# Performance work log

Hardware: AMD Instinct MI355X
Metric: run time of the kernel (lower is better)

The kernel has to match this reference:

```python
import jax, jax.numpy as jnp
import numpy as np

B, S, E, HD = 32, 1024, 768, 64
NUM_IMAGE_PATCHES = 49


def setup_inputs() -> dict:
    key = jax.random.key(0)
    ks = jax.random.split(key, 9)
    w = 0.02
    return {
        "decoder_sequence": jax.random.normal(ks[0], (B, S, E), dtype=jnp.float32),
        "Wq": jax.random.normal(ks[1], (E, HD), dtype=jnp.float32) * w,
        "bq": jnp.zeros((HD,), dtype=jnp.float32),
        "Wk": jax.random.normal(ks[2], (E, HD), dtype=jnp.float32) * w,
        "bk": jnp.zeros((HD,), dtype=jnp.float32),
        "Wv": jax.random.normal(ks[3], (E, HD), dtype=jnp.float32) * w,
        "bv": jnp.zeros((HD,), dtype=jnp.float32),
        "input_sequence_length": 975,
        "padding_mask": jax.random.randint(ks[4], (B, 1, S), 0, 2).astype(bool),
    }


def reference(decoder_sequence, Wq, bq, Wk, bk, Wv, bv, input_sequence_length, padding_mask):
    # single-head projections: [B,S,E] @ [E,HD] -> [B,S,HD]
    Q = decoder_sequence @ Wq + bq
    K = decoder_sequence @ Wk + bk
    V = decoder_sequence @ Wv + bv

    scores = jnp.einsum('bid,bjd->bij', Q, K) / jnp.sqrt(jnp.float32(HD))

    # mask: image-patch rows (i < 49) fully unmasked; text region is causal
    # (mask[49:,49:] = triu(-inf, diag=1)), i.e. -inf where i >= 49 and j > i.
    i = jnp.arange(S)[:, None]
    j = jnp.arange(S)[None, :]
    causal_bad = (i >= NUM_IMAGE_PATCHES) & (j > i)  # [S,S]
    scores = jnp.where(causal_bad[None, :, :], -jnp.inf, scores)

    # padding mask on keys, broadcast over queries: [B,1,S] -> [B,S,S]
    scores = jnp.where(padding_mask, -jnp.inf, scores)

    A = jax.nn.softmax(scores, axis=-1)
    H = jnp.einsum('bij,bjd->bid', A, V)
    return H
```

## Files before the change

kernel.cpp:

```cpp
#include <hip/hip_runtime.h>
#include <stdint.h>
#include <stddef.h>


typedef __attribute__((ext_vector_type(8))) short bf16x8;
typedef __attribute__((ext_vector_type(4))) float f32x4;

#define NIP 49
#define QSCALE 0.18033688011112042f

#define GLDS16(g, l)                                      \
  __builtin_amdgcn_global_load_lds(                       \
      (const __attribute__((address_space(1))) void*)(g), \
      (__attribute__((address_space(3))) void*)(l), 16, 0, 0)

__device__ __forceinline__ short f2b(float f) {
  union { float f; uint32_t u; } c; c.f = f;
  uint32_t u = c.u;
  uint32_t r = (u + 0x7fffu + ((u >> 16) & 1u)) >> 16;
  return (short)(uint16_t)r;
}

__device__ __forceinline__ uint32_t pk2(float lo, float hi) {
  uint32_t r;
  asm("v_cvt_pk_bf16_f32 %0, %1, %2" : "=v"(r) : "v"(lo), "v"(hi));
  return r;
}

__global__ __launch_bounds__(256) void wt_kernel(
    const float* __restrict__ Wq, const float* __restrict__ Wk,
    const float* __restrict__ Wv, const int* __restrict__ pad,
    short* __restrict__ Wt, float* __restrict__ padneg) {
  int idx = blockIdx.x * 256 + threadIdx.x;
  int n = idx / 768;
  int k = idx - n * 768;
  const float* W = (n < 64) ? Wq : (n < 128) ? Wk : Wv;
  Wt[idx] = f2b(W[(size_t)k * 64 + (n & 63)]);
  if (idx < 32768) padneg[idx] = pad[idx] ? -16384.f : 0.f;
}

__global__ __launch_bounds__(256, 3) void proj_kernel(
    const float* __restrict__ X, const float* __restrict__ bq,
    const float* __restrict__ bk, const float* __restrict__ bv,
    const short* __restrict__ Wt, short* __restrict__ Qg,
    short* __restrict__ Kg, short* __restrict__ Vt) {
  __shared__ short lW[2][2][192][32];
  const int tid = threadIdx.x;
  const int wid = tid >> 6, lane = tid & 63;
  const int l15 = lane & 15, q4 = lane >> 4;
  const int r0 = blockIdx.x * 64;
  const int sig = (l15 >> 1) & 3;

  const float* xrow = X + (size_t)(r0 + wid * 16 + l15) * 768;
  float4 xa[2][4];
  auto xload = [&](int slot, int st) {
    const int kb = st * 64 + q4 * 8;
#pragma unroll
    for (int h = 0; h < 2; ++h) {
      xa[slot][h * 2 + 0] = *(const float4*)(xrow + kb + h * 32);
      xa[slot][h * 2 + 1] = *(const float4*)(xrow + kb + h * 32 + 4);
    }
  };
  auto mkfrag = [&](int slot, int h) {
    union { uint32_t u[4]; bf16x8 v; } r;
    const float4 a = xa[slot][h * 2], b = xa[slot][h * 2 + 1];
    r.u[0] = pk2(a.x, a.y); r.u[1] = pk2(a.z, a.w);
    r.u[2] = pk2(b.x, b.y); r.u[3] = pk2(b.z, b.w);
    return r.v;
  };

  const int wr = lane >> 2;
  const int ws = (((lane & 3) ^ ((wr >> 1) & 3)) * 8);
  auto wlds = [&](int buf, int st) {
    const int kb = st * 64;
#pragma unroll
    for (int i = 0; i < 6; ++i) {
      const int fi = wid * 6 + i;
      const int j = fi >> 1, ks = fi & 1;
      GLDS16(Wt + (size_t)(j * 16 + wr) * 768 + kb + ks * 32 + ws,
             &lW[buf][ks][j * 16][0]);
    }
  };

  f32x4 acc[12];
#pragma unroll
  for (int c = 0; c < 12; ++c) acc[c] = (f32x4){0.f, 0.f, 0.f, 0.f};

  wlds(0, 0);
  __builtin_amdgcn_sched_barrier(0);
  xload(0, 0);
  xload(1, 1);
  asm volatile("s_waitcnt vmcnt(8) lgkmcnt(0)" ::: "memory");
  __builtin_amdgcn_s_barrier();

#pragma unroll
  for (int st = 0; st < 12; ++st) {
    const int cur = st & 1;
    if (st + 1 < 12) {
      wlds(cur ^ 1, st + 1);
      __builtin_amdgcn_sched_barrier(0);
    }
    const bf16x8 a0 = mkfrag(cur, 0);
    const bf16x8 a1 = mkfrag(cur, 1);
    if (st + 2 < 12) xload(cur, st + 2);
#pragma unroll
    for (int ks = 0; ks < 2; ++ks) {
      const bf16x8 a = ks ? a1 : a0;
#pragma unroll
      for (int c = 0; c < 12; ++c) {
        const bf16x8 bw =
            *(const bf16x8*)&lW[cur][ks][c * 16 + l15][(q4 ^ sig) * 8];
        acc[c] = __builtin_amdgcn_mfma_f32_16x16x32_bf16(a, bw, acc[c], 0, 0, 0);
      }
    }
    if (st + 2 < 12)
      asm volatile("s_waitcnt vmcnt(4) lgkmcnt(0)" ::: "memory");
    else
      asm volatile("s_waitcnt vmcnt(0) lgkmcnt(0)" ::: "memory");
    __builtin_amdgcn_s_barrier();
  }

  const int b = r0 >> 10, s0 = r0 & 1023;
#pragma unroll
  for (int c = 0; c < 12; ++c) {
    const int mtx = c >> 2;
    const int h = (c & 3) * 16 + l15;
    if (mtx < 2) {
      const float bias = (mtx == 0 ? bq : bk)[h];
      short* op = (mtx == 0) ? Qg : Kg;
#pragma unroll
      for (int rr = 0; rr < 4; ++rr) {
        int row = r0 + wid * 16 + q4 * 4 + rr;
        float v = acc[c][rr] + bias;
        if (mtx == 0) v *= QSCALE;
        op[(size_t)row * 64 + h] = f2b(v);
      }
    } else {
      const float bias = bv[h];
      uint2 sv;
      sv.x = pk2(acc[c][0] + bias, acc[c][1] + bias);
      sv.y = pk2(acc[c][2] + bias, acc[c][3] + bias);
      *(uint2*)(Vt + ((size_t)(b * 64 + h) << 10) + s0 + wid * 16 + q4 * 4) = sv;
    }
  }
}

__global__ __launch_bounds__(256, 2) void attn_kernel(
    const short* __restrict__ Qg, const short* __restrict__ Kg,
    const short* __restrict__ Vt, const float* __restrict__ padneg,
    float* __restrict__ out) {
  __shared__ short lK[2][2][128][32];
  __shared__ short lV[2][4][64][32];
  __shared__ short lOnes[16][32];

  const int b = blockIdx.x;
  const int level = blockIdx.y;
  const int t = (level == 0) ? 0 : 16 - level;
  const int tid = threadIdx.x;
  const int wid = tid >> 6, lane = tid & 63;
  const int l15 = lane & 15, q4 = lane >> 4;
  const int qs = t * 64;
  const size_t base = (size_t)b * 1024;
  const int nkt = (t == 0) ? 8 : (t / 2 + 1);

  {
    int i0 = tid, i1 = tid + 256;
    ((short*)lOnes)[i0] = ((i0 >> 5) == 0) ? (short)0x3F80 : (short)0;
    if (i1 < 512) ((short*)lOnes)[i1] = ((i1 >> 5) == 0) ? (short)0x3F80 : (short)0;
  }

  const short* qrow = Qg + (base + qs + wid * 16 + l15) * 64;
  bf16x8 bq0 = *(const bf16x8*)(qrow + q4 * 8);
  bf16x8 bq1 = *(const bf16x8*)(qrow + 32 + q4 * 8);
  const int qi = qs + wid * 16 + l15;

  const int sr = lane >> 2, sc = (lane & 3) * 8;
  auto wlds_tile = [&](int buf, int kt) {
    const int kb = kt * 128;
#pragma unroll
    for (int i = 0; i < 4; ++i) {
      const int dh = i & 1, krow = wid * 32 + (i >> 1) * 16;
      GLDS16(Kg + (base + kb + krow + sr) * 64 + dh * 32 + sc,
             &lK[buf][dh][krow][0]);
    }
#pragma unroll
    for (int kq = 0; kq < 4; ++kq) {
      GLDS16(Vt + ((size_t)(b * 64 + wid * 16 + sr) << 10) + kb + kq * 32 + sc,
             &lV[buf][kq][wid * 16][0]);
    }
  };

  float4 pnv[8];
  auto pnload = [&](int kt) {
#pragma unroll
    for (int c = 0; c < 8; ++c)
      pnv[c] = *(const float4*)(padneg + base + kt * 128 + c * 16 + q4 * 4);
  };

  pnload(0);
  wlds_tile(0, 0);
  __syncthreads();

  f32x4 o[5];
#pragma unroll
  for (int c = 0; c < 5; ++c) o[c] = (f32x4){0.f, 0.f, 0.f, 0.f};

  for (int kt = 0; kt < nkt; ++kt) {
    const int cur = kt & 1;
    const int kb = kt * 128;

    f32x4 s4[8];
#pragma unroll
    for (int c = 0; c < 8; ++c)
      s4[c] = (f32x4){pnv[c].x, pnv[c].y, pnv[c].z, pnv[c].w};

    if (kt + 1 < nkt) {
      wlds_tile(cur ^ 1, kt + 1);
      pnload(kt + 1);
    }

#pragma unroll
    for (int c = 0; c < 8; ++c) {
      bf16x8 a0 = *(const bf16x8*)&lK[cur][0][c * 16 + l15][q4 * 8];
      s4[c] = __builtin_amdgcn_mfma_f32_16x16x32_bf16(a0, bq0, s4[c], 0, 0, 0);
      bf16x8 a1 = *(const bf16x8*)&lK[cur][1][c * 16 + l15][q4 * 8];
      s4[c] = __builtin_amdgcn_mfma_f32_16x16x32_bf16(a1, bq1, s4[c], 0, 0, 0);
    }

    const bool diag = (t == 0) ? (kt == 0) : (kt == nkt - 1);
    const bool img = (t == 0 && kt > 0);
#pragma unroll
    for (int c = 0; c < 8; ++c) {
#pragma unroll
      for (int rr = 0; rr < 4; ++rr) {
        float pv = exp2f(fminf(s4[c][rr], 80.f));
        if (diag) {
          int j = kb + c * 16 + q4 * 4 + rr;
          if (qi >= NIP && j > qi) pv = 0.f;
        }
        if (img) {
          if (qi >= NIP) pv = 0.f;
        }
        s4[c][rr] = pv;
      }
    }

#pragma unroll
    for (int m = 0; m < 4; ++m) {
      uint32_t w0 = pk2(s4[2 * m][0], s4[2 * m][1]);
      uint32_t w1 = pk2(s4[2 * m][2], s4[2 * m][3]);
      uint32_t w2 = pk2(s4[2 * m + 1][0], s4[2 * m + 1][1]);
      uint32_t w3 = pk2(s4[2 * m + 1][2], s4[2 * m + 1][3]);
      asm("v_permlane32_swap_b32 %0, %1" : "+v"(w0), "+v"(w2));
      asm("v_permlane32_swap_b32 %0, %1" : "+v"(w1), "+v"(w3));
      asm("v_permlane16_swap_b32 %0, %1" : "+v"(w0), "+v"(w2));
      asm("v_permlane16_swap_b32 %0, %1" : "+v"(w1), "+v"(w3));
      union { uint32_t u[4]; bf16x8 v; } af;
      af.u[0] = w0; af.u[1] = w1; af.u[2] = w2; af.u[3] = w3;
#pragma unroll
      for (int c = 0; c < 5; ++c) {
        bf16x8 bv = (c < 4) ? *(const bf16x8*)&lV[cur][m][c * 16 + l15][q4 * 8]
                            : *(const bf16x8*)&lOnes[l15][q4 * 8];
        o[c] = __builtin_amdgcn_mfma_f32_16x16x32_bf16(af.v, bv, o[c], 0, 0, 0);
      }
    }
    __syncthreads();
  }

#pragma unroll
  for (int rr = 0; rr < 4; ++rr) {
    float l = __shfl(o[4][rr], lane & 48, 64);
    const float inv = (l > 0.f) ? 1.0f / l : 0.f;
    const size_t row = base + qs + wid * 16 + q4 * 4 + rr;
#pragma unroll
    for (int c = 0; c < 4; ++c)
      out[row * 64 + c * 16 + l15] = o[c][rr] * inv;
  }
}

extern "C" void kernel_launch(void* const* d_in, const int* in_sizes, int n_in,
                              void* d_out, int out_size, void* d_ws, size_t ws_size,
                              hipStream_t stream) {
  const float* X  = (const float*)d_in[0];
  const float* Wq = (const float*)d_in[1];
  const float* bq = (const float*)d_in[2];
  const float* Wk = (const float*)d_in[3];
  const float* bk = (const float*)d_in[4];
  const float* Wv = (const float*)d_in[5];
  const float* bv = (const float*)d_in[6];
  const int* pad  = (const int*)d_in[8];
  float* out = (float*)d_out;

  short* Qg = (short*)d_ws;
  short* Kg = Qg + 32768 * 64;
  short* Vt = Kg + 32768 * 64;
  short* Wt = Vt + 32768 * 64;
  float* padneg = (float*)(Wt + 147456);

  wt_kernel<<<576, 256, 0, stream>>>(Wq, Wk, Wv, pad, Wt, padneg);
  proj_kernel<<<512, 256, 0, stream>>>(X, bq, bk, bv, Wt, Qg, Kg, Vt);
  attn_kernel<<<dim3(32, 16), 256, 0, stream>>>(Qg, Kg, Vt, padneg, out);
}
```

Measured before the change: 198.1 us.

## Load projection weights directly from global memory instead of LDS staging

The projection kernel no longer stages the transposed weight tiles in shared memory with async global-to-LDS loads, double buffering and barriers. Each wave now reads its bf16 weight fragments straight from global memory, relying on L1/L2 caching because every block reuses the same small weight matrix. The weight transpose kernel is rewritten to read the source coalesced and scatter-write the transpose, and the occupancy hint on launch_bounds is dropped. This removes LDS traffic and block-wide synchronisation but exposes global load latency inside the MFMA loop with no explicit prefetch.

```diff
diff --git a/kernel.cpp b/kernel.cpp
--- a/kernel.cpp
+++ b/kernel.cpp
@@ -32,24 +32,23 @@
     const float* __restrict__ Wv, const int* __restrict__ pad,
     short* __restrict__ Wt, float* __restrict__ padneg) {
   int idx = blockIdx.x * 256 + threadIdx.x;
-  int n = idx / 768;
-  int k = idx - n * 768;
-  const float* W = (n < 64) ? Wq : (n < 128) ? Wk : Wv;
-  Wt[idx] = f2b(W[(size_t)k * 64 + (n & 63)]);
+  int m = idx / 49152;
+  int idx2 = idx - m * 49152;
+  int k = idx2 >> 6, n = idx2 & 63;
+  const float* W = (m == 0) ? Wq : (m == 1) ? Wk : Wv;
+  Wt[(size_t)(m * 64 + n) * 768 + k] = f2b(W[idx2]);
   if (idx < 32768) padneg[idx] = pad[idx] ? -16384.f : 0.f;
 }
 
-__global__ __launch_bounds__(256, 3) void proj_kernel(
+__global__ __launch_bounds__(256) void proj_kernel(
     const float* __restrict__ X, const float* __restrict__ bq,
     const float* __restrict__ bk, const float* __restrict__ bv,
     const short* __restrict__ Wt, short* __restrict__ Qg,
     short* __restrict__ Kg, short* __restrict__ Vt) {
-  __shared__ short lW[2][2][192][32];
   const int tid = threadIdx.x;
   const int wid = tid >> 6, lane = tid & 63;
   const int l15 = lane & 15, q4 = lane >> 4;
   const int r0 = blockIdx.x * 64;
-  const int sig = (l15 >> 1) & 3;
 
   const float* xrow = X + (size_t)(r0 + wid * 16 + l15) * 768;
   float4 xa[2][4];
@@ -69,55 +68,29 @@
     return r.v;
   };
 
-  const int wr = lane >> 2;
-  const int ws = (((lane & 3) ^ ((wr >> 1) & 3)) * 8);
-  auto wlds = [&](int buf, int st) {
-    const int kb = st * 64;
-#pragma unroll
-    for (int i = 0; i < 6; ++i) {
-      const int fi = wid * 6 + i;
-      const int j = fi >> 1, ks = fi & 1;
-      GLDS16(Wt + (size_t)(j * 16 + wr) * 768 + kb + ks * 32 + ws,
-             &lW[buf][ks][j * 16][0]);
-    }
-  };
+  const short* wrow = Wt + (size_t)l15 * 768 + q4 * 8;
 
   f32x4 acc[12];
 #pragma unroll
   for (int c = 0; c < 12; ++c) acc[c] = (f32x4){0.f, 0.f, 0.f, 0.f};
 
-  wlds(0, 0);
-  __builtin_amdgcn_sched_barrier(0);
   xload(0, 0);
   xload(1, 1);
-  asm volatile("s_waitcnt vmcnt(8) lgkmcnt(0)" ::: "memory");
-  __builtin_amdgcn_s_barrier();
 
 #pragma unroll
   for (int st = 0; st < 12; ++st) {
     const int cur = st & 1;
-    if (st + 1 < 12) {
-      wlds(cur ^ 1, st + 1);
-      __builtin_amdgcn_sched_barrier(0);
-    }
     const bf16x8 a0 = mkfrag(cur, 0);
     const bf16x8 a1 = mkfrag(cur, 1);
     if (st + 2 < 12) xload(cur, st + 2);
 #pragma unroll
-    for (int ks = 0; ks < 2; ++ks) {
-      const bf16x8 a = ks ? a1 : a0;
-#pragma unroll
-      for (int c = 0; c < 12; ++c) {
-        const bf16x8 bw =
-            *(const bf16x8*)&lW[cur][ks][c * 16 + l15][(q4 ^ sig) * 8];
-        acc[c] = __builtin_amdgcn_mfma_f32_16x16x32_bf16(a, bw, acc[c], 0, 0, 0);
-      }
-    }
-    if (st + 2 < 12)
-      asm volatile("s_waitcnt vmcnt(4) lgkmcnt(0)" ::: "memory");
-    else
-      asm volatile("s_waitcnt vmcnt(0) lgkmcnt(0)" ::: "memory");
-    __builtin_amdgcn_s_barrier();
+    for (int c = 0; c < 12; ++c) {
+      const short* wp = wrow + (size_t)c * 12288 + st * 64;
+      const bf16x8 b0 = *(const bf16x8*)(wp);
+      const bf16x8 b1 = *(const bf16x8*)(wp + 32);
+      acc[c] = __builtin_amdgcn_mfma_f32_16x16x32_bf16(a0, b0, acc[c], 0, 0, 0);
+      acc[c] = __builtin_amdgcn_mfma_f32_16x16x32_bf16(a1, b1, acc[c], 0, 0, 0);
+    }
   }
 
   const int b = r0 >> 10, s0 = r0 & 1023;
```

Result: slower. 243.5 us (+22.9%).
